# Optimization experiments

Hardware: AMD Instinct MI355X
Metric: run time of the kernel (lower is better)

The kernel has to match this reference:

```python
import jax, jax.numpy as jnp
import numpy as np

UP = 4
INTERVAL = 4      # coarse base interval from init
SAMP_INT = 4      # sampling_interval (fine, diagonal region)
DWID = 2          # diagonal_width
K = 3             # sample_size (AutoSample conv kernel)
Q2 = float(2 ** (INTERVAL + 2)); L2 = 2 ** (8 - INTERVAL - 2) + 1   # coarse full-space LUT: 64, 5
Q1 = float(2 ** SAMP_INT);       L1 = 2 ** (8 - SAMP_INT) + 1       # fine diagonal LUT: 16, 17
DW = 2 * DWID + 1
R1 = L1 * DW * DW * DW


def round_ste(v):
    # straight-through round, as in MuLUT's round_func
    return v + jax.lax.stop_gradient(jnp.round(v) - v)


def _msb_lsb(v, q, L):
    i = jnp.clip(jnp.floor(v / q).astype(jnp.int32), 0, L - 2)
    return i, v - i.astype(v.dtype) * q


def _simplex(f, q):
    # 4D simplex (tetrahedral) interpolation weights + vertex increments.
    # f: [..., 4] LSB fractions. Sorting descending reproduces the 24-case if/else.
    order = jnp.argsort(-f, axis=-1)
    fs = jnp.take_along_axis(f, order, axis=-1)
    w = jnp.stack([q - fs[..., 0],
                   fs[..., 0] - fs[..., 1],
                   fs[..., 1] - fs[..., 2],
                   fs[..., 2] - fs[..., 3],
                   fs[..., 3]], axis=-1) / q              # [...,5]
    oh = jax.nn.one_hot(order, 4, dtype=jnp.int32)        # [...,4,4]
    inc = jnp.cumsum(oh, axis=-2)
    inc = jnp.concatenate([jnp.zeros_like(inc[..., :1, :]), inc], axis=-2)  # [...,5,4]
    return w, inc


def _interp_mode(img, sw, w1, w2, res, r2i):
    # img [N,1,H,W] in [0,255]; sw [4,1,K,K]; w1 [R1,oc] fine LUT; w2 [L2^4,oc] coarse LUT; res [oc]
    pad = K - 1
    imgp = jnp.pad(img, ((0, 0), (0, 0), (0, pad), (0, pad)), mode='edge')
    abcd = jax.lax.conv_general_dilated(imgp, sw, (1, 1), 'VALID',
                                        dimension_numbers=('NCHW', 'OIHW', 'NCHW'))
    v = jnp.clip(jnp.moveaxis(abcd, 1, -1), 0.0, 255.0)   # [N,H,W,4] sampled (a,b,c,d)
    # coarse full-space path (compress2)
    i2, f2 = _msb_lsb(v, Q2, L2)
    wgt2, inc2 = _simplex(f2, Q2)
    vert2 = jnp.clip(i2[..., None, :] + inc2, 0, L2 - 1)  # [N,H,W,5,4]
    flat2 = ((vert2[..., 0] * L2 + vert2[..., 1]) * L2 + vert2[..., 2]) * L2 + vert2[..., 3]
    out2 = jnp.einsum('...v,...vo->...o', wgt2, w2[flat2])
    # fine diagonal path (compress1 via ref2index)
    i1, f1 = _msb_lsb(v, Q1, L1)
    wgt1, inc1 = _simplex(f1, Q1)
    vert1 = jnp.clip(i1[..., None, :] + inc1, 0, L1 - 1)
    jx = vert1[..., 0]
    off = jnp.clip(vert1[..., 1:] - jx[..., None] + DWID, 0, DW - 1)
    rows = r2i[jx, off[..., 0], off[..., 1], off[..., 2]]
    out1 = jnp.einsum('...v,...vo->...o', wgt1, w1[rows])
    within = ((jnp.abs(i1[..., 1] - i1[..., 0]) <= DWID - 1) &
              (jnp.abs(i1[..., 2] - i1[..., 0]) <= DWID - 1) &
              (jnp.abs(i1[..., 3] - i1[..., 0]) <= DWID - 1))
    return jnp.where(within[..., None], out1, out2) + res  # [N,H,W,oc]


def _stage(img, sw, w1, w2, res, r2i):
    # mode x rotation ensemble; sw [M,4,1,K,K]; w1 [M,R1,oc]; w2 [M,625,oc]; res [M,oc]
    M = sw.shape[0]
    acc = 0.0
    for m in range(M):
        for r in range(4):
            xr = jnp.rot90(img, r, axes=(2, 3))
            o = _interp_mode(xr, sw[m], w1[m], w2[m], res[m], r2i)
            o = jnp.moveaxis(o, -1, 1)                    # [N,oc,h,w]
            acc = acc + jnp.rot90(o, -r, axes=(2, 3))
    return acc / (4.0 * M)


def _stage6(feat, sw, w1, w2, res, r2i):
    # feat [N,4,H,W]; sw [M,4,4,1,K,K]; w1 [M,4,R1,up^2]; res [M,4,up^2]
    M = sw.shape[0]
    acc = 0.0
    for m in range(M):
        for c in range(4):
            for r in range(4):
                xr = jnp.rot90(feat[:, c:c + 1], r, axes=(2, 3))
                o = _interp_mode(xr, sw[m, c], w1[m, c], w2[m, c], res[m, c], r2i)
                N, h, w, _ = o.shape
                # pixel shuffle before rotating back
                o = o.reshape(N, h, w, UP, UP).transpose(0, 1, 3, 2, 4).reshape(N, 1, h * UP, w * UP)
                acc = acc + jnp.rot90(o, -r, axes=(2, 3))
    return acc / (4.0 * 4.0 * M)


def setup_inputs() -> dict:
    key = jax.random.key(0)
    ks = jax.random.split(key, 14)
    B, H, W = 2, 192, 192
    x = jax.random.uniform(ks[0], (B, 1, H, W), jnp.float32)
    ref2index = jnp.arange(R1, dtype=jnp.int64).reshape(L1, DW, DW, DW)
    # samplers scaled to keep sampled pixel values roughly in [0,255]
    samp_s123 = jax.random.uniform(ks[1], (3, 3, 4, 1, K, K), jnp.float32) / (K * K)
    samp_s4 = jax.random.uniform(ks[2], (3, 4, 1, K, K), jnp.float32) / (K * K)
    samp_s6 = jax.random.uniform(ks[3], (3, 4, 4, 1, K, K), jnp.float32) / (K * K)
    w1_s123 = jax.random.normal(ks[4], (3, 3, R1, 2), jnp.float32) * 0.1
    w2_s123 = jax.random.normal(ks[5], (3, 3, L2 ** 4, 2), jnp.float32) * 0.1
    res_s123 = jax.random.normal(ks[6], (3, 3, 2), jnp.float32) * 0.01
    w1_s4 = jax.random.normal(ks[7], (3, R1, 1), jnp.float32) * 0.1
    w2_s4 = jax.random.normal(ks[8], (3, L2 ** 4, 1), jnp.float32) * 0.1
    res_s4 = jax.random.normal(ks[9], (3, 1), jnp.float32) * 0.01
    w1_s6 = jax.random.normal(ks[10], (3, 4, R1, UP * UP), jnp.float32) * 0.1
    w2_s6 = jax.random.normal(ks[11], (3, 4, L2 ** 4, UP * UP), jnp.float32) * 0.1
    res_s6 = jax.random.normal(ks[12], (3, 4, UP * UP), jnp.float32) * 0.01
    return {'x': x, 'ref2index': ref2index,
            'samp_s123': samp_s123, 'w1_s123': w1_s123, 'w2_s123': w2_s123, 'res_s123': res_s123,
            'samp_s4': samp_s4, 'w1_s4': w1_s4, 'w2_s4': w2_s4, 'res_s4': res_s4,
            'samp_s6': samp_s6, 'w1_s6': w1_s6, 'w2_s6': w2_s6, 'res_s6': res_s6}


def reference(x, ref2index, samp_s123, w1_s123, w2_s123, res_s123,
              samp_s4, w1_s4, w2_s4, res_s4,
              samp_s6, w1_s6, w2_s6, res_s6):
    cur = round_ste(jnp.clip(x * 255.0, 0.0, 255.0))
    refine = []
    for s in range(3):  # stages 1-3, out_c=2: ch0 -> refine, ch1 -> next stage
        pred = _stage(cur, samp_s123[s], w1_s123[s], w2_s123[s], res_s123[s], ref2index)
        y = round_ste(jnp.clip(pred * 255.0, 0.0, 255.0))
        refine.append(y[:, 0:1])
        cur = y[:, 1:2]
    pred = _stage(cur, samp_s4, w1_s4, w2_s4, res_s4, ref2index)  # stage 4, out_c=1
    refine.append(round_ste(jnp.clip(pred * 255.0, 0.0, 255.0)))
    feat = jnp.concatenate(refine, axis=1)  # [B,4,H,W]
    hr = _stage6(feat, samp_s6, w1_s6, w2_s6, res_s6, ref2index)  # [B,1,H*up,W*up]
    return jnp.clip(hr * 255.0, 0.0, 255.0) / 255.0
```

## Files before the change

### kernel.cpp

```cpp
#include <hip/hip_runtime.h>

#define HW   192
#define HW2  (HW*HW)
#define NPIX (2*HW2)
#define NUP  (HW*4)

__device__ __forceinline__ float clamp255f(float v){ return fminf(fmaxf(v,0.f),255.f); }

__device__ __forceinline__ void simplex_core(const float v4[4],
    bool& within_o, int idx[5], float wgt[5])
{
  float f1[4], f2[4]; int i1[4], i2[4];
#pragma unroll
  for (int k=0;k<4;k++){
    float vk = clamp255f(v4[k]);
    int a = (int)(vk*0.0625f);   a = a>15?15:a;
    int b = (int)(vk*0.015625f); b = b>3 ?3 :b;
    i1[k]=a; f1[k]=vk-(float)a*16.f;
    i2[k]=b; f2[k]=vk-(float)b*64.f;
  }
  const int d1=i1[1]-i1[0], d2=i1[2]-i1[0], d3=i1[3]-i1[0];
  const bool within = (d1<=1)&&(d1>=-1)&&(d2<=1)&&(d2>=-1)&&(d3<=1)&&(d3>=-1);
  within_o = within;

  float ff[4]; int ii[4];
#pragma unroll
  for (int k=0;k<4;k++){ ff[k]= within?f1[k]:f2[k]; ii[k]= within?i1[k]:i2[k]; }
  const float Q    = within?16.f:64.f;
  const float qinv = within?0.0625f:0.015625f;

  const int rk0 = (ff[1]> ff[0]) + (ff[2]> ff[0]) + (ff[3]> ff[0]);
  const int rk1 = (ff[0]>=ff[1]) + (ff[2]> ff[1]) + (ff[3]> ff[1]);
  const int rk2 = (ff[0]>=ff[2]) + (ff[1]>=ff[2]) + (ff[3]> ff[2]);
  const int rk3 = (ff[0]>=ff[3]) + (ff[1]>=ff[3]) + (ff[2]>=ff[3]);

  float a0=ff[0],a1=ff[1],a2=ff[2],a3=ff[3],t;
  t=fmaxf(a0,a1); a1=fminf(a0,a1); a0=t;
  t=fmaxf(a2,a3); a3=fminf(a2,a3); a2=t;
  t=fmaxf(a0,a2); a2=fminf(a0,a2); a0=t;
  t=fmaxf(a1,a3); a3=fminf(a1,a3); a1=t;
  t=fmaxf(a1,a2); a2=fminf(a1,a2); a1=t;

  wgt[0]=(Q-a0)*qinv; wgt[1]=(a0-a1)*qinv; wgt[2]=(a1-a2)*qinv;
  wgt[3]=(a2-a3)*qinv; wgt[4]=a3*qinv;

#pragma unroll
  for (int t5=0;t5<5;t5++){
    const int c0 = rk0<t5, c1 = rk1<t5, c2 = rk2<t5, c3 = rk3<t5;
    const int A0 = ii[0]+c0;
    const int A1 = within ? (d1 + c1 - c0 + 2) : (ii[1]+c1);
    const int A2 = within ? (d2 + c2 - c0 + 2) : (ii[2]+c2);
    const int A3 = within ? (d3 + c3 - c0 + 2) : (ii[3]+c3);
    idx[t5] = A0*125 + A1*25 + A2*5 + A3;
  }
}

template<int OUTC>
__device__ __forceinline__ void interp_eval(const float v4[4],
    const float* __restrict__ w1m, const float* __restrict__ w2m, float* out)
{
  bool within; int idx[5]; float wgt[5];
  simplex_core(v4, within, idx, wgt);
  float s[OUTC];
#pragma unroll
  for (int c=0;c<OUTC;c++) s[c]=0.f;
#pragma unroll
  for (int t5=0;t5<5;t5++){
    const float w = wgt[t5];
    if constexpr (OUTC==2){
      const float2 p = within ? reinterpret_cast<const float2*>(w1m)[idx[t5]]
                              : reinterpret_cast<const float2*>(w2m)[idx[t5]];
      s[0]=fmaf(w,p.x,s[0]); s[1]=fmaf(w,p.y,s[1]);
    } else {
      const float p = within ? w1m[idx[t5]] : w2m[idx[t5]];
      s[0]=fmaf(w, p, s[0]);
    }
  }
#pragma unroll
  for (int c=0;c<OUTC;c++) out[c]=s[c];
}

__device__ __forceinline__ void interp_accum16(const float v4[4],
    const float* __restrict__ w1m, const float* __restrict__ w2m, float acc[16])
{
  bool within; int idx[5]; float wgt[5];
  simplex_core(v4, within, idx, wgt);
  const float* tab = within ? w1m : w2m;
#pragma unroll
  for (int t5=0;t5<5;t5++){
    const float w = wgt[t5];
    const float4* row = reinterpret_cast<const float4*>(tab + (size_t)idx[t5]*16);
    float4 p0=row[0], p1=row[1], p2=row[2], p3=row[3];
    acc[0]=fmaf(w,p0.x,acc[0]); acc[1]=fmaf(w,p0.y,acc[1]); acc[2]=fmaf(w,p0.z,acc[2]); acc[3]=fmaf(w,p0.w,acc[3]);
    acc[4]=fmaf(w,p1.x,acc[4]); acc[5]=fmaf(w,p1.y,acc[5]); acc[6]=fmaf(w,p1.z,acc[6]); acc[7]=fmaf(w,p1.w,acc[7]);
    acc[8]=fmaf(w,p2.x,acc[8]); acc[9]=fmaf(w,p2.y,acc[9]); acc[10]=fmaf(w,p2.z,acc[10]); acc[11]=fmaf(w,p2.w,acc[11]);
    acc[12]=fmaf(w,p3.x,acc[12]); acc[13]=fmaf(w,p3.y,acc[13]); acc[14]=fmaf(w,p3.z,acc[14]); acc[15]=fmaf(w,p3.w,acc[15]);
  }
}

template<int OUTC, bool QUANT>
__global__ void __launch_bounds__(256) stage_kernel(
    const float* __restrict__ img, const float* __restrict__ sw,
    const float* __restrict__ w1,  const float* __restrict__ w2,
    const float* __restrict__ res, float* __restrict__ outA, float* __restrict__ outB)
{
  const int t   = blockIdx.x*256 + threadIdx.x;
  const int r   = t & 3;
  const int pix = t >> 2;
  if (pix >= NPIX) return;
  const int b = pix/HW2, rem = pix - b*HW2;
  const int y = rem/HW,  x   = rem - y*HW;
  const float* im = img + b*HW2;

  float tap[9];
#pragma unroll
  for (int kh=0;kh<3;kh++)
#pragma unroll
    for (int kw=0;kw<3;kw++){
      int ry = (r==0)? y+kh : (r==1)? y+kw : (r==2)? y-kh : y-kw;
      int cx = (r==0)? x+kw : (r==1)? x-kh : (r==2)? x-kw : x+kh;
      ry = min(max(ry,0),HW-1); cx = min(max(cx,0),HW-1);
      float p = im[ry*HW+cx];
      if constexpr (QUANT) p = rintf(clamp255f(p*255.f));
      tap[kh*3+kw]=p;
    }

  float pm[3][OUTC];
#pragma unroll
  for (int m=0;m<3;m++){
    const float* swm = sw + m*36;
    float v[4];
#pragma unroll
    for (int oc=0;oc<4;oc++){
      float a=0.f;
#pragma unroll
      for (int k=0;k<9;k++) a = fmaf(swm[oc*9+k], tap[k], a);
      v[oc]=a;
    }
    float o[OUTC];
    interp_eval<OUTC>(v, w1 + (size_t)m*2125*OUTC, w2 + (size_t)m*625*OUTC, o);
#pragma unroll
    for (int c=0;c<OUTC;c++) pm[m][c] = o[c] + res[m*OUTC+c];
  }

  const int lane = threadIdx.x & 63;
  const int base = lane & ~3;
  float acc[OUTC];
#pragma unroll
  for (int c=0;c<OUTC;c++) acc[c]=0.f;
#pragma unroll
  for (int m=0;m<3;m++)
#pragma unroll
    for (int rr=0;rr<4;rr++){
#pragma unroll
      for (int c=0;c<OUTC;c++) acc[c] += __shfl(pm[m][c], base+rr, 64);
    }

  if (r==0){
    outA[pix] = rintf(clamp255f((acc[0]/12.0f)*255.0f));
    if constexpr (OUTC==2)
      outB[pix] = rintf(clamp255f((acc[1]/12.0f)*255.0f));
  }
}

__global__ void __launch_bounds__(256) stage6_kernel(
    const float* __restrict__ feat, const float* __restrict__ sw,
    const float* __restrict__ w1,   const float* __restrict__ w2,
    const float* __restrict__ res,  float* __restrict__ out)
{
  __shared__ float lds[4][64][17];
  const int lane = threadIdx.x & 63;
  const int c    = threadIdx.x >> 6;
  const int r    = lane & 3;
  const int pl   = lane >> 2;
  const int pix  = blockIdx.x*16 + pl;
  const int b  = pix/HW2, rem = pix - b*HW2;
  const int by = rem/HW,  bx  = rem - by*HW;

  const float* im = feat + (size_t)c*NPIX + b*HW2;
  float tap[9];
#pragma unroll
  for (int kh=0;kh<3;kh++)
#pragma unroll
    for (int kw=0;kw<3;kw++){
      int ry = (r==0)? by+kh : (r==1)? by+kw : (r==2)? by-kh : by-kw;
      int cx = (r==0)? bx+kw : (r==1)? bx-kh : (r==2)? bx-kw : bx+kh;
      ry = min(max(ry,0),HW-1); cx = min(max(cx,0),HW-1);
      tap[kh*3+kw] = im[ry*HW+cx];
    }

  float racc[16];
#pragma unroll
  for (int i=0;i<16;i++) racc[i]=0.f;

#pragma unroll
  for (int m=0;m<3;m++){
    const int mc = m*4 + c;
    const float* swmc = sw + mc*36;
    float v[4];
#pragma unroll
    for (int oc=0;oc<4;oc++){
      float a=0.f;
#pragma unroll
      for (int k=0;k<9;k++) a = fmaf(swmc[oc*9+k], tap[k], a);
      v[oc]=a;
    }
    const float* remc = res + mc*16;
#pragma unroll
    for (int i=0;i<16;i++) racc[i] += remc[i];
    interp_accum16(v, w1 + (size_t)mc*2125*16, w2 + (size_t)mc*625*16, racc);
  }

#pragma unroll
  for (int i=0;i<16;i++) lds[c][lane][i] = racc[i];
  __syncthreads();

  if (c == 0){
    float s[16];
#pragma unroll
    for (int i=0;i<16;i++)
      s[i] = ((lds[0][lane][i] + lds[1][lane][i]) + lds[2][lane][i]) + lds[3][lane][i];

    float po[16];
    if (r==0){
#pragma unroll
      for (int i=0;i<16;i++) po[i]=s[i];
    } else if (r==1){
#pragma unroll
      for (int p=0;p<4;p++)
#pragma unroll
        for (int q=0;q<4;q++) po[p*4+q]=s[(3-q)*4+p];
    } else if (r==2){
#pragma unroll
      for (int p=0;p<4;p++)
#pragma unroll
        for (int q=0;q<4;q++) po[p*4+q]=s[(3-p)*4+(3-q)];
    } else {
#pragma unroll
      for (int p=0;p<4;p++)
#pragma unroll
        for (int q=0;q<4;q++) po[p*4+q]=s[q*4+(3-p)];
    }

#pragma unroll
    for (int i=0;i<16;i++){
      po[i] += __shfl_xor(po[i],1);
      po[i] += __shfl_xor(po[i],2);
    }

    auto fin = [](float sv)->float{
      const float hr = sv/48.0f;
      return fminf(fmaxf(hr*255.f,0.f),255.f)/255.f;
    };
    float* op = out + (size_t)b*(NUP*NUP) + (size_t)(4*by+r)*NUP + 4*bx;
    *reinterpret_cast<float4*>(op) =
        make_float4(fin(po[r*4+0]),fin(po[r*4+1]),fin(po[r*4+2]),fin(po[r*4+3]));
  }
}

extern "C" void kernel_launch(void* const* d_in, const int* in_sizes, int n_in,
                              void* d_out, int out_size, void* d_ws, size_t ws_size,
                              hipStream_t stream)
{
  const float* x       = (const float*)d_in[0];
  const float* samp123 = (const float*)d_in[2];
  const float* w1123   = (const float*)d_in[3];
  const float* w2123   = (const float*)d_in[4];
  const float* res123  = (const float*)d_in[5];
  const float* samp4   = (const float*)d_in[6];
  const float* w14     = (const float*)d_in[7];
  const float* w24     = (const float*)d_in[8];
  const float* res4    = (const float*)d_in[9];
  const float* samp6   = (const float*)d_in[10];
  const float* w16     = (const float*)d_in[11];
  const float* w26     = (const float*)d_in[12];
  const float* res6    = (const float*)d_in[13];

  float* ws   = (float*)d_ws;
  float* feat = ws;
  float* curA = ws + 4*NPIX;
  float* curB = ws + 5*NPIX;

  const int GS = NPIX*4/256;
  const int G6 = NPIX/16;

  stage_kernel<2,true ><<<GS,256,0,stream>>>(x,    samp123,      w1123,        w2123,       res123,    feat,        curB);
  stage_kernel<2,false><<<GS,256,0,stream>>>(curB, samp123+108,  w1123+12750,  w2123+3750,  res123+6,  feat+NPIX,   curA);
  stage_kernel<2,false><<<GS,256,0,stream>>>(curA, samp123+216,  w1123+25500,  w2123+7500,  res123+12, feat+2*NPIX, curB);
  stage_kernel<1,false><<<GS,256,0,stream>>>(curB, samp4,        w14,          w24,         res4,      feat+3*NPIX, nullptr);
  stage6_kernel<<<G6,256,0,stream>>>(feat, samp6, w16, w26, res6, (float*)d_out);
}
```

Before: 179.2 us.

## Split stage6 LUT row gathers across quad lanes using ds_swizzle broadcasts

```diff
diff --git a/kernel.cpp b/kernel.cpp
--- a/kernel.cpp
+++ b/kernel.cpp
@@ -6,6 +6,15 @@
 #define NUP  (HW*4)
 
 __device__ __forceinline__ float clamp255f(float v){ return fminf(fmaxf(v,0.f),255.f); }
+
+template<int J>
+__device__ __forceinline__ int qb_i(int v){
+  return __builtin_amdgcn_ds_swizzle(v, 0x8000 + 0x55*J);
+}
+template<int J>
+__device__ __forceinline__ float qb_f(float v){
+  return __int_as_float(qb_i<J>(__float_as_int(v)));
+}
 
 __device__ __forceinline__ void simplex_core(const float v4[4],
     bool& within_o, int idx[5], float wgt[5])
@@ -80,24 +89,6 @@
   for (int c=0;c<OUTC;c++) out[c]=s[c];
 }
 
-__device__ __forceinline__ void interp_accum16(const float v4[4],
-    const float* __restrict__ w1m, const float* __restrict__ w2m, float acc[16])
-{
-  bool within; int idx[5]; float wgt[5];
-  simplex_core(v4, within, idx, wgt);
-  const float* tab = within ? w1m : w2m;
-#pragma unroll
-  for (int t5=0;t5<5;t5++){
-    const float w = wgt[t5];
-    const float4* row = reinterpret_cast<const float4*>(tab + (size_t)idx[t5]*16);
-    float4 p0=row[0], p1=row[1], p2=row[2], p3=row[3];
-    acc[0]=fmaf(w,p0.x,acc[0]); acc[1]=fmaf(w,p0.y,acc[1]); acc[2]=fmaf(w,p0.z,acc[2]); acc[3]=fmaf(w,p0.w,acc[3]);
-    acc[4]=fmaf(w,p1.x,acc[4]); acc[5]=fmaf(w,p1.y,acc[5]); acc[6]=fmaf(w,p1.z,acc[6]); acc[7]=fmaf(w,p1.w,acc[7]);
-    acc[8]=fmaf(w,p2.x,acc[8]); acc[9]=fmaf(w,p2.y,acc[9]); acc[10]=fmaf(w,p2.z,acc[10]); acc[11]=fmaf(w,p2.w,acc[11]);
-    acc[12]=fmaf(w,p3.x,acc[12]); acc[13]=fmaf(w,p3.y,acc[13]); acc[14]=fmaf(w,p3.z,acc[14]); acc[15]=fmaf(w,p3.w,acc[15]);
-  }
-}
-
 template<int OUTC, bool QUANT>
 __global__ void __launch_bounds__(256) stage_kernel(
     const float* __restrict__ img, const float* __restrict__ sw,
@@ -176,6 +167,7 @@
   const int pix  = blockIdx.x*16 + pl;
   const int b  = pix/HW2, rem = pix - b*HW2;
   const int by = rem/HW,  bx  = rem - by*HW;
+  const int r4 = r*4;
 
   const float* im = feat + (size_t)c*NPIX + b*HW2;
   float tap[9];
@@ -189,9 +181,11 @@
       tap[kh*3+kw] = im[ry*HW+cx];
     }
 
-  float racc[16];
-#pragma unroll
-  for (int i=0;i<16;i++) racc[i]=0.f;
+  float acc[4][4];
+#pragma unroll
+  for (int j=0;j<4;j++)
+#pragma unroll
+    for (int k=0;k<4;k++) acc[j][k]=0.f;
 
 #pragma unroll
   for (int m=0;m<3;m++){
@@ -207,19 +201,55 @@
     }
     const float* remc = res + mc*16;
 #pragma unroll
-    for (int i=0;i<16;i++) racc[i] += remc[i];
-    interp_accum16(v, w1 + (size_t)mc*2125*16, w2 + (size_t)mc*625*16, racc);
-  }
-
-#pragma unroll
-  for (int i=0;i<16;i++) lds[c][lane][i] = racc[i];
+    for (int j=0;j<4;j++)
+#pragma unroll
+      for (int k=0;k<4;k++) acc[j][k] += remc[r4+k];
+
+    bool within; int idx[5]; float wgt[5];
+    simplex_core(v, within, idx, wgt);
+
+    const float* w1mc = w1 + (size_t)mc*2125*16;
+    const float* w2mc = w2 + (size_t)mc*625*16;
+    const int iwv = within ? 1 : 0;
+    const int iw0=qb_i<0>(iwv), iw1=qb_i<1>(iwv), iw2=qb_i<2>(iwv), iw3=qb_i<3>(iwv);
+    const float* tb0 = iw0 ? w1mc : w2mc;
+    const float* tb1 = iw1 ? w1mc : w2mc;
+    const float* tb2 = iw2 ? w1mc : w2mc;
+    const float* tb3 = iw3 ? w1mc : w2mc;
+
+#pragma unroll
+    for (int t5=0;t5<5;t5++){
+      const int i0=qb_i<0>(idx[t5]), i1=qb_i<1>(idx[t5]), i2=qb_i<2>(idx[t5]), i3=qb_i<3>(idx[t5]);
+      const float u0=qb_f<0>(wgt[t5]), u1=qb_f<1>(wgt[t5]), u2=qb_f<2>(wgt[t5]), u3=qb_f<3>(wgt[t5]);
+      const float4 p0 = *reinterpret_cast<const float4*>(tb0 + (size_t)i0*16 + r4);
+      const float4 p1 = *reinterpret_cast<const float4*>(tb1 + (size_t)i1*16 + r4);
+      const float4 p2 = *reinterpret_cast<const float4*>(tb2 + (size_t)i2*16 + r4);
+      const float4 p3 = *reinterpret_cast<const float4*>(tb3 + (size_t)i3*16 + r4);
+      acc[0][0]=fmaf(u0,p0.x,acc[0][0]); acc[0][1]=fmaf(u0,p0.y,acc[0][1]);
+      acc[0][2]=fmaf(u0,p0.z,acc[0][2]); acc[0][3]=fmaf(u0,p0.w,acc[0][3]);
+      acc[1][0]=fmaf(u1,p1.x,acc[1][0]); acc[1][1]=fmaf(u1,p1.y,acc[1][1]);
+      acc[1][2]=fmaf(u1,p1.z,acc[1][2]); acc[1][3]=fmaf(u1,p1.w,acc[1][3]);
+      acc[2][0]=fmaf(u2,p2.x,acc[2][0]); acc[2][1]=fmaf(u2,p2.y,acc[2][1]);
+      acc[2][2]=fmaf(u2,p2.z,acc[2][2]); acc[2][3]=fmaf(u2,p2.w,acc[2][3]);
+      acc[3][0]=fmaf(u3,p3.x,acc[3][0]); acc[3][1]=fmaf(u3,p3.y,acc[3][1]);
+      acc[3][2]=fmaf(u3,p3.z,acc[3][2]); acc[3][3]=fmaf(u3,p3.w,acc[3][3]);
+    }
+  }
+
+#pragma unroll
+  for (int j=0;j<4;j++)
+#pragma unroll
+    for (int k=0;k<4;k++) lds[c][lane][j*4+k] = acc[j][k];
   __syncthreads();
 
   if (c == 0){
     float s[16];
 #pragma unroll
-    for (int i=0;i<16;i++)
-      s[i] = ((lds[0][lane][i] + lds[1][lane][i]) + lds[2][lane][i]) + lds[3][lane][i];
+    for (int i=0;i<16;i++){
+      const int row = (pl<<2) + (i>>2);
+      const int col = r4 + (i&3);
+      s[i] = ((lds[0][row][col] + lds[1][row][col]) + lds[2][row][col]) + lds[3][row][col];
+    }
 
     float po[16];
     if (r==0){
```

Measured after the change: 174.4 us. -2.7%, faster.
